# Performance work log

Hardware: AMD Instinct MI355X
Metric: run time of the kernel (lower is better)

## Reference

```python
import jax, jax.numpy as jnp
import numpy as np

N, E = 50000, 800000
IN, H = 128, 128
NTYPE, NSCHOOL, NTIME, NAUTHOR = 20, 30, 15, 200


def setup_inputs() -> dict:
    key = jax.random.key(0)
    ks = jax.random.split(key, 20)

    def lin(k, i, o):  # kaiming-ish init
        return jax.random.normal(k, (i, o), jnp.float32) * (1.0 / np.sqrt(i))

    return {
        "x0": jax.random.normal(ks[0], (N, IN), jnp.float32),
        "edge_index": jax.random.randint(ks[1], (2, E), 0, N, dtype=jnp.int64),
        # GCNConv weights (x @ W + b after aggregation)
        "W1": lin(ks[2], IN, H),   "b1": jnp.zeros((H,), jnp.float32),
        "Wt": lin(ks[3], H, NTYPE),    "bt": jnp.zeros((NTYPE,), jnp.float32),
        "Ws": lin(ks[4], H, NSCHOOL), "bs": jnp.zeros((NSCHOOL,), jnp.float32),
        "Wa": lin(ks[5], H, NAUTHOR), "ba": jnp.zeros((NAUTHOR,), jnp.float32),
        # classification heads (Linear stored as [in, out])
        "Wct": lin(ks[6], NTYPE, NTYPE),       "bct": jnp.zeros((NTYPE,), jnp.float32),
        "Wcs": lin(ks[7], NSCHOOL, NSCHOOL), "bcs": jnp.zeros((NSCHOOL,), jnp.float32),
        "Wtf": lin(ks[8], IN, NTIME),          "btf": jnp.zeros((NTIME,), jnp.float32),
        "Wca": lin(ks[9], NAUTHOR, NAUTHOR), "bca": jnp.zeros((NAUTHOR,), jnp.float32),
    }


def reference(x0, edge_index, W1, b1, Wt, bt, Ws, bs, Wa, ba,
              Wct, bct, Wcs, bcs, Wtf, btf, Wca, bca):
    n = x0.shape[0]
    src, dst = edge_index[0], edge_index[1]
    # GCNConv default: add self-loops, symmetric deg^{-1/2} normalization
    loop = jnp.arange(n, dtype=edge_index.dtype)
    src_f = jnp.concatenate([src, loop])  # [E+N]
    dst_f = jnp.concatenate([dst, loop])
    deg = jax.ops.segment_sum(jnp.ones(src_f.shape[0], jnp.float32), dst_f, num_segments=n)
    dinv = jnp.where(deg > 0, jax.lax.rsqrt(deg), 0.0)
    norm = dinv[src_f] * dinv[dst_f]  # [E+N]

    def conv(x, W, b):
        xt = x @ W                                   # transform first (small out dim)
        msg = xt[src_f] * norm[:, None]              # [E+N, out]
        return jax.ops.segment_sum(msg, dst_f, num_segments=n) + b

    h = jax.nn.relu(conv(x0, W1, b1))  # dropout is identity at inference

    out_type = jax.nn.softmax(conv(h, Wt, bt) @ Wct + bct, axis=-1)
    out_school = jax.nn.softmax(conv(h, Ws, bs) @ Wcs + bcs, axis=-1)
    out_time = jax.nn.softmax(x0 @ Wtf + btf, axis=-1)  # head reads x0 directly
    out_author = jax.nn.softmax(conv(h, Wa, ba) @ Wca + bca, axis=-1)
    return (out_type, out_school, out_time, out_author)
```

## Files before the change

kernel.cpp:

```cpp
#include <hip/hip_runtime.h>
#include <math.h>


typedef short short8 __attribute__((ext_vector_type(8)));
typedef float f32x4 __attribute__((ext_vector_type(4)));

#define FILL_CHUNK 2048

static __device__ __forceinline__ unsigned short f2bf(float x) {
  unsigned u = __float_as_uint(x);
  u += 0x7fff + ((u >> 16) & 1);
  return (unsigned short)(u >> 16);
}
static __device__ __forceinline__ unsigned pack2bf(float lo, float hi) {
  return ((unsigned)f2bf(hi) << 16) | (unsigned)f2bf(lo);
}
static __device__ __forceinline__ float bflo(unsigned u) {
  return __uint_as_float(u << 16);
}
static __device__ __forceinline__ float bfhi(unsigned u) {
  return __uint_as_float(u & 0xffff0000u);
}

__global__ __launch_bounds__(256) void k_deg_x(
    const int* __restrict__ dst, int E, int* __restrict__ deg, int rlen) {
  int rng = blockIdx.x & 7;
  int chunk = blockIdx.x >> 3;
  int lo = rng * rlen, hi = lo + rlen;
  int base = chunk * FILL_CHUNK;
  int end = base + FILL_CHUNK;
  if (end > E) end = E;
  for (int e = base + threadIdx.x; e < end; e += 256) {
    int d = dst[e];
    if (d >= lo && d < hi) atomicAdd(&deg[d], 1);
  }
}

__global__ void k_scan1(const int* __restrict__ deg, int n,
                        int* __restrict__ excl, int* __restrict__ bsum) {
  __shared__ int sm[256];
  int i = blockIdx.x * 256 + threadIdx.x;
  int v = (i < n) ? deg[i] : 0;
  sm[threadIdx.x] = v;
  __syncthreads();
#pragma unroll
  for (int o = 1; o < 256; o <<= 1) {
    int t = (threadIdx.x >= o) ? sm[threadIdx.x - o] : 0;
    __syncthreads();
    sm[threadIdx.x] += t;
    __syncthreads();
  }
  if (i < n) excl[i] = sm[threadIdx.x] - v;
  if (threadIdx.x == 255) bsum[blockIdx.x] = sm[255];
}

__global__ void k_scan2(int* __restrict__ bsum, int nb) {
  __shared__ int sm[256];
  int v = (threadIdx.x < nb) ? bsum[threadIdx.x] : 0;
  sm[threadIdx.x] = v;
  __syncthreads();
#pragma unroll
  for (int o = 1; o < 256; o <<= 1) {
    int t = (threadIdx.x >= o) ? sm[threadIdx.x - o] : 0;
    __syncthreads();
    sm[threadIdx.x] += t;
    __syncthreads();
  }
  if (threadIdx.x < nb) bsum[threadIdx.x] = sm[threadIdx.x] - v;
}

__global__ __launch_bounds__(256) void k_finscale(
    const float* __restrict__ X, const int* __restrict__ deg,
    const int* __restrict__ bsum, int* __restrict__ row_off,
    int* __restrict__ cursor, float* __restrict__ dinv,
    unsigned* __restrict__ Y, int n) {
  int p = blockIdx.x * 256 + threadIdx.x;
  if (p >= n * 64) return;
  int row = p >> 6;
  float d = rsqrtf((float)(deg[row] + 1));
  if ((p & 63) == 0) {
    int ro = row_off[row] + bsum[row >> 8];
    row_off[row] = ro;
    cursor[row] = ro;
    dinv[row] = d;
  }
  float2 v = reinterpret_cast<const float2*>(X)[p];
  Y[p] = pack2bf(v.x * d, v.y * d);
}

__global__ __launch_bounds__(256) void k_fill_x(
    const int* __restrict__ src, const int* __restrict__ dst, int E,
    int* __restrict__ cursor, unsigned short* __restrict__ csr, int rlen) {
  int rng = blockIdx.x & 7;
  int chunk = blockIdx.x >> 3;
  int lo = rng * rlen, hi = lo + rlen;
  int base = chunk * FILL_CHUNK;
  int end = base + FILL_CHUNK;
  if (end > E) end = E;
  for (int e = base + threadIdx.x; e < end; e += 256) {
    int d = dst[e];
    if (d >= lo && d < hi) {
      int p = atomicAdd(&cursor[d], 1);
      csr[p] = (unsigned short)src[e];
    }
  }
}

__global__ __launch_bounds__(256) void k_agg(
    const unsigned* __restrict__ Y, unsigned* __restrict__ out,
    const int* __restrict__ row_off, const int* __restrict__ deg,
    const unsigned short* __restrict__ csr, const float* __restrict__ dinv,
    int n) {
  int wave = threadIdx.x >> 6;
  int lane = threadIdx.x & 63;
  int sub = lane >> 5;
  int sl = lane & 31;
  int i = blockIdx.x * 8 + wave * 2 + sub;
  if (i >= n) return;
  int start = row_off[i];
  int cnt = deg[i];
  const uint2* Yv = reinterpret_cast<const uint2*>(Y);
  float a0 = 0.f, a1 = 0.f, a2 = 0.f, a3 = 0.f;
  int j = 0;
  for (; j + 3 < cnt; j += 4) {
    int s0 = csr[start + j];
    int s1 = csr[start + j + 1];
    int s2 = csr[start + j + 2];
    int s3 = csr[start + j + 3];
    uint2 u0 = Yv[(size_t)s0 * 32 + sl];
    uint2 u1 = Yv[(size_t)s1 * 32 + sl];
    uint2 u2 = Yv[(size_t)s2 * 32 + sl];
    uint2 u3 = Yv[(size_t)s3 * 32 + sl];
    a0 += (bflo(u0.x) + bflo(u1.x)) + (bflo(u2.x) + bflo(u3.x));
    a1 += (bfhi(u0.x) + bfhi(u1.x)) + (bfhi(u2.x) + bfhi(u3.x));
    a2 += (bflo(u0.y) + bflo(u1.y)) + (bflo(u2.y) + bflo(u3.y));
    a3 += (bfhi(u0.y) + bfhi(u1.y)) + (bfhi(u2.y) + bfhi(u3.y));
  }
  for (; j < cnt; ++j) {
    int s0 = csr[start + j];
    uint2 u0 = Yv[(size_t)s0 * 32 + sl];
    a0 += bflo(u0.x);
    a1 += bfhi(u0.x);
    a2 += bflo(u0.y);
    a3 += bfhi(u0.y);
  }
  uint2 us = Yv[(size_t)i * 32 + sl];
  float di = dinv[i];
  uint2 r;
  r.x = pack2bf((a0 + bflo(us.x)) * di, (a1 + bfhi(us.x)) * di);
  r.y = pack2bf((a2 + bflo(us.y)) * di, (a3 + bfhi(us.y)) * di);
  reinterpret_cast<uint2*>(out)[(size_t)i * 32 + sl] = r;
}

__global__ void k_fusepack(
    const float* __restrict__ Wt, const float* __restrict__ bt,
    const float* __restrict__ Wct, const float* __restrict__ bct,
    const float* __restrict__ Ws, const float* __restrict__ bs,
    const float* __restrict__ Wcs, const float* __restrict__ bcs,
    const float* __restrict__ Wa, const float* __restrict__ ba,
    const float* __restrict__ Wca, const float* __restrict__ bca,
    unsigned short* __restrict__ WfPk, float* __restrict__ bf,
    const float* __restrict__ W1, unsigned short* __restrict__ W1Pk) {
  if (blockIdx.x >= 256) {
    int t = (blockIdx.x - 256) * 128 + threadIdx.x;
    int i = t >> 7, c = t & 127;
    W1Pk[((i >> 3) * 128 + c) * 8 + (i & 7)] = f2bf(W1[t]);
    return;
  }
  int c = blockIdx.x;
  int i = threadIdx.x;
  float acc = 0.f, bacc = 0.f;
  if (c < 20) {
    for (int k = 0; k < 20; ++k) {
      float w2 = Wct[k * 20 + c];
      acc += Wt[i * 20 + k] * w2;
      bacc += bt[k] * w2;
    }
    bacc += bct[c];
  } else if (c < 50) {
    int cc = c - 20;
    for (int k = 0; k < 30; ++k) {
      float w2 = Wcs[k * 30 + cc];
      acc += Ws[i * 30 + k] * w2;
      bacc += bs[k] * w2;
    }
    bacc += bcs[cc];
  } else if (c < 250) {
    int cc = c - 50;
    for (int k = 0; k < 200; ++k) {
      float w2 = Wca[k * 200 + cc];
      acc += Wa[i * 200 + k] * w2;
      bacc += ba[k] * w2;
    }
    bacc += bca[cc];
  }
  WfPk[((i >> 3) * 256 + c) * 8 + (i & 7)] = f2bf(acc);
  if (i == 0) bf[c] = bacc;
}

static __device__ __forceinline__ void stage32(
    const short* __restrict__ A, short (*sAb)[136], int rowBase, int n, int tid) {
  for (int t = tid; t < 32 * 16; t += 256) {
    int r = t >> 4, c8 = t & 15;
    int gr = rowBase + r;
    short8 v = (short8){0, 0, 0, 0, 0, 0, 0, 0};
    if (gr < n) v = *reinterpret_cast<const short8*>(A + (size_t)gr * 128 + c8 * 8);
    *reinterpret_cast<short8*>(&sAb[r][c8 * 8]) = v;
  }
}

__global__ __launch_bounds__(256) void k_mfma_gemm128(
    const short* __restrict__ A, const unsigned short* __restrict__ Wpk,
    const float* __restrict__ bias, const float* __restrict__ dinv,
    unsigned short* __restrict__ out, int n) {
  __shared__ short sAb[32][136];
  int rowBase = blockIdx.x * 32;
  stage32(A, sAb, rowBase, n, threadIdx.x);
  __syncthreads();
  int wave = threadIdx.x >> 6, lane = threadIdx.x & 63;
  int rg = wave >> 1, ch = wave & 1;
  int lr = lane & 15, lg = lane >> 4;
  int r0 = rowBase + rg * 16;
  short8 afr[4];
#pragma unroll
  for (int kk = 0; kk < 4; ++kk)
    afr[kk] = *reinterpret_cast<const short8*>(&sAb[rg * 16 + lr][kk * 32 + lg * 8]);
  f32x4 acc[4];
#pragma unroll
  for (int t = 0; t < 4; ++t) acc[t] = (f32x4){0.f, 0.f, 0.f, 0.f};
  const short8* Wp8 = reinterpret_cast<const short8*>(Wpk);
#pragma unroll
  for (int t = 0; t < 4; ++t) {
#pragma unroll
    for (int kk = 0; kk < 4; ++kk) {
      short8 bfr = Wp8[(kk * 4 + lg) * 128 + ch * 64 + t * 16 + lr];
      acc[t] = __builtin_amdgcn_mfma_f32_16x16x32_bf16(afr[kk], bfr, acc[t], 0, 0, 0);
    }
  }
  int rloc = r0 + lg * 4;
#pragma unroll
  for (int t = 0; t < 4; ++t) {
    int col = ch * 64 + t * 16 + lr;
    float b = bias[col];
#pragma unroll
    for (int reg = 0; reg < 4; ++reg) {
      int row = rloc + reg;
      if (row < n) {
        float v = fmaxf(acc[t][reg] + b, 0.f) * dinv[row];
        out[(size_t)row * 128 + col] = f2bf(v);
      }
    }
  }
}

__global__ __launch_bounds__(256) void k_heads_fused(
    const short* __restrict__ A, const unsigned short* __restrict__ Wpk,
    const float* __restrict__ bf, float* __restrict__ outT,
    float* __restrict__ outS, float* __restrict__ outA, int n) {
  __shared__ short sAb[32][136];
  __shared__ float aM[2][2][16];
  __shared__ float aS[2][2][16];
  int rowBase = blockIdx.x * 32;
  stage32(A, sAb, rowBase, n, threadIdx.x);
  __syncthreads();
  int wave = threadIdx.x >> 6, lane = threadIdx.x & 63;
  int rg = wave >> 1, ch = wave & 1;
  int lr = lane & 15, lg = lane >> 4;
  int r0 = rowBase + rg * 16;
  int cb = ch * 128;
  short8 afr[4];
#pragma unroll
  for (int kk = 0; kk < 4; ++kk)
    afr[kk] = *reinterpret_cast<const short8*>(&sAb[rg * 16 + lr][kk * 32 + lg * 8]);
  f32x4 acc[8];
#pragma unroll
  for (int t = 0; t < 8; ++t) acc[t] = (f32x4){0.f, 0.f, 0.f, 0.f};
  const short8* Wp8 = reinterpret_cast<const short8*>(Wpk);
#pragma unroll
  for (int t = 0; t < 8; ++t) {
#pragma unroll
    for (int kk = 0; kk < 4; ++kk) {
      short8 bfr = Wp8[(kk * 4 + lg) * 256 + cb + t * 16 + lr];
      acc[t] = __builtin_amdgcn_mfma_f32_16x16x32_bf16(afr[kk], bfr, acc[t], 0, 0, 0);
    }
  }
  float bias_l[8];
#pragma unroll
  for (int t = 0; t < 8; ++t) bias_l[t] = bf[cb + t * 16 + lr];
  float mTr[4], mSr[4], mAr[4];
#pragma unroll
  for (int reg = 0; reg < 4; ++reg) {
    float mT = -INFINITY, mS = -INFINITY, mA = -INFINITY;
#pragma unroll
    for (int t = 0; t < 8; ++t) {
      int c = cb + t * 16 + lr;
      float val = acc[t][reg] + bias_l[t];
      acc[t][reg] = val;
      if (c < 20) mT = fmaxf(mT, val);
      else if (c < 50) mS = fmaxf(mS, val);
      else if (c < 250) mA = fmaxf(mA, val);
    }
#pragma unroll
    for (int o = 8; o; o >>= 1) {
      mT = fmaxf(mT, __shfl_xor(mT, o, 64));
      mS = fmaxf(mS, __shfl_xor(mS, o, 64));
      mA = fmaxf(mA, __shfl_xor(mA, o, 64));
    }
    mTr[reg] = mT; mSr[reg] = mS; mAr[reg] = mA;
    if (lr == 0) aM[rg][ch][lg * 4 + reg] = mA;
  }
  __syncthreads();
#pragma unroll
  for (int reg = 0; reg < 4; ++reg)
    mAr[reg] = fmaxf(mAr[reg], aM[rg][ch ^ 1][lg * 4 + reg]);
  float sTr[4], sSr[4], sAr[4];
#pragma unroll
  for (int reg = 0; reg < 4; ++reg) {
    float sT = 0.f, sS = 0.f, sA = 0.f;
#pragma unroll
    for (int t = 0; t < 8; ++t) {
      int c = cb + t * 16 + lr;
      float m = (c < 20) ? mTr[reg] : (c < 50) ? mSr[reg] : mAr[reg];
      float e = __expf(acc[t][reg] - m);
      acc[t][reg] = e;
      if (c < 20) sT += e;
      else if (c < 50) sS += e;
      else if (c < 250) sA += e;
    }
#pragma unroll
    for (int o = 8; o; o >>= 1) {
      sT += __shfl_xor(sT, o, 64);
      sS += __shfl_xor(sS, o, 64);
      sA += __shfl_xor(sA, o, 64);
    }
    sTr[reg] = sT; sSr[reg] = sS; sAr[reg] = sA;
    if (lr == 0) aS[rg][ch][lg * 4 + reg] = sA;
  }
  __syncthreads();
#pragma unroll
  for (int reg = 0; reg < 4; ++reg)
    sAr[reg] += aS[rg][ch ^ 1][lg * 4 + reg];
  int rloc = r0 + lg * 4;
#pragma unroll
  for (int reg = 0; reg < 4; ++reg) {
    int row = rloc + reg;
    if (row >= n) continue;
    float iT = 1.f / sTr[reg], iS = 1.f / sSr[reg], iA = 1.f / sAr[reg];
#pragma unroll
    for (int t = 0; t < 8; ++t) {
      int c = cb + t * 16 + lr;
      float e = acc[t][reg];
      if (c < 20) outT[(size_t)row * 20 + c] = e * iT;
      else if (c < 50) outS[(size_t)row * 30 + (c - 20)] = e * iS;
      else if (c < 250) outA[(size_t)row * 200 + (c - 50)] = e * iA;
    }
  }
}

__global__ __launch_bounds__(256) void k_time(
    const float* __restrict__ x0, const float* __restrict__ Wtf,
    const float* __restrict__ btf, float* __restrict__ outT, int n) {
  __shared__ float sW[128][16];
  __shared__ float sb[16];
  for (int t = threadIdx.x; t < 128 * 16; t += 256) {
    int k = t >> 4, j = t & 15;
    sW[k][j] = (j < 15) ? Wtf[k * 15 + j] : 0.f;
  }
  if (threadIdx.x < 16) sb[threadIdx.x] = (threadIdx.x < 15) ? btf[threadIdx.x] : 0.f;
  __syncthreads();
  int j = threadIdx.x & 15;
  int rl = threadIdx.x >> 4;
  int r = blockIdx.x * 16 + rl;
  if (r >= n) return;
  float acc = sb[j];
  const float4* xr = reinterpret_cast<const float4*>(x0 + (size_t)r * 128);
  for (int k4 = 0; k4 < 32; ++k4) {
    float4 xv = xr[k4];
    acc += xv.x * sW[k4 * 4 + 0][j] + xv.y * sW[k4 * 4 + 1][j] +
           xv.z * sW[k4 * 4 + 2][j] + xv.w * sW[k4 * 4 + 3][j];
  }
  float m = (j < 15) ? acc : -INFINITY;
#pragma unroll
  for (int o = 8; o; o >>= 1) m = fmaxf(m, __shfl_xor(m, o, 16));
  float e = (j < 15) ? __expf(acc - m) : 0.f;
  float s = e;
#pragma unroll
  for (int o = 8; o; o >>= 1) s += __shfl_xor(s, o, 16);
  if (j < 15) outT[(size_t)r * 15 + j] = e / s;
}

extern "C" void kernel_launch(void* const* d_in, const int* in_sizes, int n_in,
                              void* d_out, int out_size, void* d_ws, size_t ws_size,
                              hipStream_t stream) {
  const float* x0 = (const float*)d_in[0];
  const int* ei = (const int*)d_in[1];
  const float* W1 = (const float*)d_in[2];
  const float* b1 = (const float*)d_in[3];
  const float* Wt = (const float*)d_in[4];
  const float* bt = (const float*)d_in[5];
  const float* Ws = (const float*)d_in[6];
  const float* bs = (const float*)d_in[7];
  const float* Wa = (const float*)d_in[8];
  const float* ba = (const float*)d_in[9];
  const float* Wct = (const float*)d_in[10];
  const float* bct = (const float*)d_in[11];
  const float* Wcs = (const float*)d_in[12];
  const float* bcs = (const float*)d_in[13];
  const float* Wtf = (const float*)d_in[14];
  const float* btf = (const float*)d_in[15];
  const float* Wca = (const float*)d_in[16];
  const float* bca = (const float*)d_in[17];
  (void)n_in; (void)out_size; (void)ws_size;

  int N = in_sizes[0] / 128;
  int E = in_sizes[1] / 2;
  float* out = (float*)d_out;

  char* ws = (char*)d_ws;
  size_t off = 0;
  auto alloc = [&](size_t bytes) -> void* {
    void* p = ws + off;
    off = (off + bytes + 255) & ~(size_t)255;
    return p;
  };
  int* deg = (int*)alloc((size_t)N * 4);
  int* row_off = (int*)alloc((size_t)N * 4);
  int* bsum = (int*)alloc(256 * 4);
  int* cursor = (int*)alloc((size_t)N * 4);
  float* dinv = (float*)alloc((size_t)N * 4);
  unsigned short* csr = (unsigned short*)alloc((size_t)E * 2);
  unsigned short* WfPk = (unsigned short*)alloc((size_t)128 * 256 * 2);
  unsigned short* W1Pk = (unsigned short*)alloc((size_t)128 * 128 * 2);
  float* bf = (float*)alloc(256 * 4);
  unsigned* Yb = (unsigned*)alloc((size_t)N * 64 * 4);
  unsigned* Ab = (unsigned*)alloc((size_t)N * 64 * 4);
  unsigned* Bb = (unsigned*)alloc((size_t)N * 64 * 4);

  const int* srcp = ei;
  const int* dstp = ei + E;
  int gN = (N + 255) / 256;
  int g32 = (N + 31) / 32;
  int rlen = (N + 7) / 8;
  int gX = 8 * ((E + FILL_CHUNK - 1) / FILL_CHUNK);

  hipMemsetAsync(deg, 0, (size_t)N * 4, stream);
  k_deg_x<<<gX, 256, 0, stream>>>(dstp, E, deg, rlen);
  k_scan1<<<gN, 256, 0, stream>>>(deg, N, row_off, bsum);
  k_scan2<<<1, 256, 0, stream>>>(bsum, gN);
  k_finscale<<<(N * 64 + 255) / 256, 256, 0, stream>>>(
      x0, deg, bsum, row_off, cursor, dinv, Yb, N);
  k_fill_x<<<gX, 256, 0, stream>>>(srcp, dstp, E, cursor, csr, rlen);
  k_fusepack<<<384, 128, 0, stream>>>(Wt, bt, Wct, bct, Ws, bs, Wcs, bcs, Wa, ba,
                                      Wca, bca, WfPk, bf, W1, W1Pk);
  k_agg<<<(N + 7) / 8, 256, 0, stream>>>(Yb, Ab, row_off, deg, csr, dinv, N);
  k_mfma_gemm128<<<g32, 256, 0, stream>>>(
      (const short*)Ab, W1Pk, b1, dinv, (unsigned short*)Bb, N);
  k_agg<<<(N + 7) / 8, 256, 0, stream>>>(Bb, Ab, row_off, deg, csr, dinv, N);
  k_heads_fused<<<g32, 256, 0, stream>>>(
      (const short*)Ab, WfPk, bf, out, out + (size_t)N * 20, out + (size_t)N * 65, N);
  k_time<<<(N + 15) / 16, 256, 0, stream>>>(x0, Wtf, btf, out + (size_t)N * 50, N);
}
```

Before: 336.8 us.

## Fuse neighbor aggregation into GEMM kernels, merge time head, simplify CSR build

The sparse aggregation now writes straight into the shared-memory A tile of the following MFMA GEMM and heads kernels, so the intermediate aggregated feature buffer no longer goes through global memory and two launches are dropped. The time-head softmax runs as extra blocks of the heads kernel and reads Wtf directly instead of staging it in LDS. The range-partitioned degree and fill kernels are replaced by simple one-thread-per-edge atomic kernels. Each GEMM block now does 32 rows of irregular gathers before its MFMA phase, which may lower latency hiding. Unpartitioned atomics may also contend more or lose locality.

```diff
diff --git a/kernel.cpp b/kernel.cpp
--- a/kernel.cpp
+++ b/kernel.cpp
@@ -4,8 +4,6 @@
 
 typedef short short8 __attribute__((ext_vector_type(8)));
 typedef float f32x4 __attribute__((ext_vector_type(4)));
-
-#define FILL_CHUNK 2048
 
 static __device__ __forceinline__ unsigned short f2bf(float x) {
   unsigned u = __float_as_uint(x);
@@ -22,18 +20,9 @@
   return __uint_as_float(u & 0xffff0000u);
 }
 
-__global__ __launch_bounds__(256) void k_deg_x(
-    const int* __restrict__ dst, int E, int* __restrict__ deg, int rlen) {
-  int rng = blockIdx.x & 7;
-  int chunk = blockIdx.x >> 3;
-  int lo = rng * rlen, hi = lo + rlen;
-  int base = chunk * FILL_CHUNK;
-  int end = base + FILL_CHUNK;
-  if (end > E) end = E;
-  for (int e = base + threadIdx.x; e < end; e += 256) {
-    int d = dst[e];
-    if (d >= lo && d < hi) atomicAdd(&deg[d], 1);
-  }
+__global__ void k_deg(const int* __restrict__ dst, int E, int* __restrict__ deg) {
+  int e = blockIdx.x * blockDim.x + threadIdx.x;
+  if (e < E) atomicAdd(&deg[dst[e]], 1);
 }
 
 __global__ void k_scan1(const int* __restrict__ deg, int n,
@@ -88,68 +77,15 @@
   Y[p] = pack2bf(v.x * d, v.y * d);
 }
 
-__global__ __launch_bounds__(256) void k_fill_x(
-    const int* __restrict__ src, const int* __restrict__ dst, int E,
-    int* __restrict__ cursor, unsigned short* __restrict__ csr, int rlen) {
-  int rng = blockIdx.x & 7;
-  int chunk = blockIdx.x >> 3;
-  int lo = rng * rlen, hi = lo + rlen;
-  int base = chunk * FILL_CHUNK;
-  int end = base + FILL_CHUNK;
-  if (end > E) end = E;
-  for (int e = base + threadIdx.x; e < end; e += 256) {
+__global__ void k_fill(const int* __restrict__ src, const int* __restrict__ dst,
+                       int E, int* __restrict__ cursor,
+                       unsigned short* __restrict__ csr) {
+  int e = blockIdx.x * blockDim.x + threadIdx.x;
+  if (e < E) {
     int d = dst[e];
-    if (d >= lo && d < hi) {
-      int p = atomicAdd(&cursor[d], 1);
-      csr[p] = (unsigned short)src[e];
-    }
-  }
-}
-
-__global__ __launch_bounds__(256) void k_agg(
-    const unsigned* __restrict__ Y, unsigned* __restrict__ out,
-    const int* __restrict__ row_off, const int* __restrict__ deg,
-    const unsigned short* __restrict__ csr, const float* __restrict__ dinv,
-    int n) {
-  int wave = threadIdx.x >> 6;
-  int lane = threadIdx.x & 63;
-  int sub = lane >> 5;
-  int sl = lane & 31;
-  int i = blockIdx.x * 8 + wave * 2 + sub;
-  if (i >= n) return;
-  int start = row_off[i];
-  int cnt = deg[i];
-  const uint2* Yv = reinterpret_cast<const uint2*>(Y);
-  float a0 = 0.f, a1 = 0.f, a2 = 0.f, a3 = 0.f;
-  int j = 0;
-  for (; j + 3 < cnt; j += 4) {
-    int s0 = csr[start + j];
-    int s1 = csr[start + j + 1];
-    int s2 = csr[start + j + 2];
-    int s3 = csr[start + j + 3];
-    uint2 u0 = Yv[(size_t)s0 * 32 + sl];
-    uint2 u1 = Yv[(size_t)s1 * 32 + sl];
-    uint2 u2 = Yv[(size_t)s2 * 32 + sl];
-    uint2 u3 = Yv[(size_t)s3 * 32 + sl];
-    a0 += (bflo(u0.x) + bflo(u1.x)) + (bflo(u2.x) + bflo(u3.x));
-    a1 += (bfhi(u0.x) + bfhi(u1.x)) + (bfhi(u2.x) + bfhi(u3.x));
-    a2 += (bflo(u0.y) + bflo(u1.y)) + (bflo(u2.y) + bflo(u3.y));
-    a3 += (bfhi(u0.y) + bfhi(u1.y)) + (bfhi(u2.y) + bfhi(u3.y));
-  }
-  for (; j < cnt; ++j) {
-    int s0 = csr[start + j];
-    uint2 u0 = Yv[(size_t)s0 * 32 + sl];
-    a0 += bflo(u0.x);
-    a1 += bfhi(u0.x);
-    a2 += bflo(u0.y);
-    a3 += bfhi(u0.y);
-  }
-  uint2 us = Yv[(size_t)i * 32 + sl];
-  float di = dinv[i];
-  uint2 r;
-  r.x = pack2bf((a0 + bflo(us.x)) * di, (a1 + bfhi(us.x)) * di);
-  r.y = pack2bf((a2 + bflo(us.y)) * di, (a3 + bfhi(us.y)) * di);
-  reinterpret_cast<uint2*>(out)[(size_t)i * 32 + sl] = r;
+    int p = atomicAdd(&cursor[d], 1);
+    csr[p] = (unsigned short)src[e];
+  }
 }
 
 __global__ void k_fusepack(
@@ -198,24 +134,66 @@
   if (i == 0) bf[c] = bacc;
 }
 
-static __device__ __forceinline__ void stage32(
-    const short* __restrict__ A, short (*sAb)[136], int rowBase, int n, int tid) {
-  for (int t = tid; t < 32 * 16; t += 256) {
-    int r = t >> 4, c8 = t & 15;
-    int gr = rowBase + r;
-    short8 v = (short8){0, 0, 0, 0, 0, 0, 0, 0};
-    if (gr < n) v = *reinterpret_cast<const short8*>(A + (size_t)gr * 128 + c8 * 8);
-    *reinterpret_cast<short8*>(&sAb[r][c8 * 8]) = v;
-  }
-}
-
-__global__ __launch_bounds__(256) void k_mfma_gemm128(
-    const short* __restrict__ A, const unsigned short* __restrict__ Wpk,
-    const float* __restrict__ bias, const float* __restrict__ dinv,
-    unsigned short* __restrict__ out, int n) {
+static __device__ __forceinline__ void agg_to_lds(
+    const unsigned* __restrict__ Y, short (*sAb)[136], int rowBase,
+    const int* __restrict__ row_off, const int* __restrict__ deg,
+    const unsigned short* __restrict__ csr, const float* __restrict__ dinv,
+    int n, int tid) {
+  int wave = tid >> 6, lane = tid & 63;
+  int sub = lane >> 5, sl = lane & 31;
+  const uint2* Yv = reinterpret_cast<const uint2*>(Y);
+#pragma unroll
+  for (int it = 0; it < 4; ++it) {
+    int r = wave * 8 + it * 2 + sub;
+    int i = rowBase + r;
+    uint2 rr;
+    if (i < n) {
+      int start = row_off[i];
+      int cnt = deg[i];
+      float a0 = 0.f, a1 = 0.f, a2 = 0.f, a3 = 0.f;
+      int j = 0;
+      for (; j + 3 < cnt; j += 4) {
+        int s0 = csr[start + j];
+        int s1 = csr[start + j + 1];
+        int s2 = csr[start + j + 2];
+        int s3 = csr[start + j + 3];
+        uint2 u0 = Yv[(size_t)s0 * 32 + sl];
+        uint2 u1 = Yv[(size_t)s1 * 32 + sl];
+        uint2 u2 = Yv[(size_t)s2 * 32 + sl];
+        uint2 u3 = Yv[(size_t)s3 * 32 + sl];
+        a0 += (bflo(u0.x) + bflo(u1.x)) + (bflo(u2.x) + bflo(u3.x));
+        a1 += (bfhi(u0.x) + bfhi(u1.x)) + (bfhi(u2.x) + bfhi(u3.x));
+        a2 += (bflo(u0.y) + bflo(u1.y)) + (bflo(u2.y) + bflo(u3.y));
+        a3 += (bfhi(u0.y) + bfhi(u1.y)) + (bfhi(u2.y) + bfhi(u3.y));
+      }
+      for (; j < cnt; ++j) {
+        int s0 = csr[start + j];
+        uint2 u0 = Yv[(size_t)s0 * 32 + sl];
+        a0 += bflo(u0.x);
+        a1 += bfhi(u0.x);
+        a2 += bflo(u0.y);
+        a3 += bfhi(u0.y);
+      }
+      uint2 us = Yv[(size_t)i * 32 + sl];
+      float di = dinv[i];
+      rr.x = pack2bf((a0 + bflo(us.x)) * di, (a1 + bfhi(us.x)) * di);
+      rr.y = pack2bf((a2 + bflo(us.y)) * di, (a3 + bfhi(us.y)) * di);
+    } else {
+      rr.x = 0u;
+      rr.y = 0u;
+    }
+    *reinterpret_cast<uint2*>(&sAb[r][sl * 4]) = rr;
+  }
+}
+
+__global__ __launch_bounds__(256) void k_agg_gemm128(
+    const unsigned* __restrict__ Y, const int* __restrict__ row_off,
+    const int* __restrict__ deg, const unsigned short* __restrict__ csr,
+    const float* __restrict__ dinv, const unsigned short* __restrict__ Wpk,
+    const float* __restrict__ bias, unsigned short* __restrict__ out, int n) {
   __shared__ short sAb[32][136];
   int rowBase = blockIdx.x * 32;
-  stage32(A, sAb, rowBase, n, threadIdx.x);
+  agg_to_lds(Y, sAb, rowBase, row_off, deg, csr, dinv, n, threadIdx.x);
   __syncthreads();
   int wave = threadIdx.x >> 6, lane = threadIdx.x & 63;
   int rg = wave >> 1, ch = wave & 1;
@@ -253,15 +231,44 @@
   }
 }
 
-__global__ __launch_bounds__(256) void k_heads_fused(
-    const short* __restrict__ A, const unsigned short* __restrict__ Wpk,
-    const float* __restrict__ bf, float* __restrict__ outT,
-    float* __restrict__ outS, float* __restrict__ outA, int n) {
+__global__ __launch_bounds__(256) void k_agg_heads_time(
+    const unsigned* __restrict__ Y, const int* __restrict__ row_off,
+    const int* __restrict__ deg, const unsigned short* __restrict__ csr,
+    const float* __restrict__ dinv, const unsigned short* __restrict__ Wpk,
+    const float* __restrict__ bfb, const float* __restrict__ x0,
+    const float* __restrict__ Wtf, const float* __restrict__ btf,
+    float* __restrict__ outT, float* __restrict__ outS,
+    float* __restrict__ outTime, float* __restrict__ outA, int n) {
+  int g32 = (n + 31) / 32;
+  if ((int)blockIdx.x >= g32) {
+    int tb = blockIdx.x - g32;
+    int j = threadIdx.x & 15;
+    int rl = threadIdx.x >> 4;
+    int r = tb * 16 + rl;
+    if (r >= n) return;
+    int jj = (j < 15) ? j : 14;
+    float acc = btf[jj];
+    const float4* xr = reinterpret_cast<const float4*>(x0 + (size_t)r * 128);
+    for (int k4 = 0; k4 < 32; ++k4) {
+      float4 xv = xr[k4];
+      acc += xv.x * Wtf[(k4 * 4 + 0) * 15 + jj] + xv.y * Wtf[(k4 * 4 + 1) * 15 + jj] +
+             xv.z * Wtf[(k4 * 4 + 2) * 15 + jj] + xv.w * Wtf[(k4 * 4 + 3) * 15 + jj];
+    }
+    float m = (j < 15) ? acc : -INFINITY;
+#pragma unroll
+    for (int o = 8; o; o >>= 1) m = fmaxf(m, __shfl_xor(m, o, 16));
+    float e = (j < 15) ? __expf(acc - m) : 0.f;
+    float s = e;
+#pragma unroll
+    for (int o = 8; o; o >>= 1) s += __shfl_xor(s, o, 16);
+    if (j < 15) outTime[(size_t)r * 15 + j] = e / s;
+    return;
+  }
   __shared__ short sAb[32][136];
   __shared__ float aM[2][2][16];
   __shared__ float aS[2][2][16];
   int rowBase = blockIdx.x * 32;
-  stage32(A, sAb, rowBase, n, threadIdx.x);
+  agg_to_lds(Y, sAb, rowBase, row_off, deg, csr, dinv, n, threadIdx.x);
   __syncthreads();
   int wave = threadIdx.x >> 6, lane = threadIdx.x & 63;
   int rg = wave >> 1, ch = wave & 1;
@@ -286,7 +293,7 @@
   }
   float bias_l[8];
 #pragma unroll
-  for (int t = 0; t < 8; ++t) bias_l[t] = bf[cb + t * 16 + lr];
+  for (int t = 0; t < 8; ++t) bias_l[t] = bfb[cb + t * 16 + lr];
   float mTr[4], mSr[4], mAr[4];
 #pragma unroll
   for (int reg = 0; reg < 4; ++reg) {
@@ -355,38 +362,6 @@
       else if (c < 250) outA[(size_t)row * 200 + (c - 50)] = e * iA;
     }
   }
-}
-
-__global__ __launch_bounds__(256) void k_time(
-    const float* __restrict__ x0, const float* __restrict__ Wtf,
-    const float* __restrict__ btf, float* __restrict__ outT, int n) {
-  __shared__ float sW[128][16];
-  __shared__ float sb[16];
-  for (int t = threadIdx.x; t < 128 * 16; t += 256) {
-    int k = t >> 4, j = t & 15;
-    sW[k][j] = (j < 15) ? Wtf[k * 15 + j] : 0.f;
-  }
-  if (threadIdx.x < 16) sb[threadIdx.x] = (threadIdx.x < 15) ? btf[threadIdx.x] : 0.f;
-  __syncthreads();
-  int j = threadIdx.x & 15;
-  int rl = threadIdx.x >> 4;
-  int r = blockIdx.x * 16 + rl;
-  if (r >= n) return;
-  float acc = sb[j];
-  const float4* xr = reinterpret_cast<const float4*>(x0 + (size_t)r * 128);
-  for (int k4 = 0; k4 < 32; ++k4) {
-    float4 xv = xr[k4];
-    acc += xv.x * sW[k4 * 4 + 0][j] + xv.y * sW[k4 * 4 + 1][j] +
-           xv.z * sW[k4 * 4 + 2][j] + xv.w * sW[k4 * 4 + 3][j];
-  }
-  float m = (j < 15) ? acc : -INFINITY;
-#pragma unroll
-  for (int o = 8; o; o >>= 1) m = fmaxf(m, __shfl_xor(m, o, 16));
-  float e = (j < 15) ? __expf(acc - m) : 0.f;
-  float s = e;
-#pragma unroll
-  for (int o = 8; o; o >>= 1) s += __shfl_xor(s, o, 16);
-  if (j < 15) outT[(size_t)r * 15 + j] = e / s;
 }
 
 extern "C" void kernel_launch(void* const* d_in, const int* in_sizes, int n_in,
@@ -431,32 +406,29 @@
   unsigned short* csr = (unsigned short*)alloc((size_t)E * 2);
   unsigned short* WfPk = (unsigned short*)alloc((size_t)128 * 256 * 2);
   unsigned short* W1Pk = (unsigned short*)alloc((size_t)128 * 128 * 2);
-  float* bf = (float*)alloc(256 * 4);
+  float* bfb = (float*)alloc(256 * 4);
   unsigned* Yb = (unsigned*)alloc((size_t)N * 64 * 4);
-  unsigned* Ab = (unsigned*)alloc((size_t)N * 64 * 4);
   unsigned* Bb = (unsigned*)alloc((size_t)N * 64 * 4);
 
   const int* srcp = ei;
   const int* dstp = ei + E;
+  int gE = (E + 255) / 256;
   int gN = (N + 255) / 256;
   int g32 = (N + 31) / 32;
-  int rlen = (N + 7) / 8;
-  int gX = 8 * ((E + FILL_CHUNK - 1) / FILL_CHUNK);
+  int gT = (N + 15) / 16;
 
   hipMemsetAsync(deg, 0, (size_t)N * 4, stream);
-  k_deg_x<<<gX, 256, 0, stream>>>(dstp, E, deg, rlen);
+  k_deg<<<gE, 256, 0, stream>>>(dstp, E, deg);
   k_scan1<<<gN, 256, 0, stream>>>(deg, N, row_off, bsum);
   k_scan2<<<1, 256, 0, stream>>>(bsum, gN);
   k_finscale<<<(N * 64 + 255) / 256, 256, 0, stream>>>(
       x0, deg, bsum, row_off, cursor, dinv, Yb, N);
-  k_fill_x<<<gX, 256, 0, stream>>>(srcp, dstp, E, cursor, csr, rlen);
+  k_fill<<<gE, 256, 0, stream>>>(srcp, dstp, E, cursor, csr);
   k_fusepack<<<384, 128, 0, stream>>>(Wt, bt, Wct, bct, Ws, bs, Wcs, bcs, Wa, ba,
-                                      Wca, bca, WfPk, bf, W1, W1Pk);
-  k_agg<<<(N + 7) / 8, 256, 0, stream>>>(Yb, Ab, row_off, deg, csr, dinv, N);
-  k_mfma_gemm128<<<g32, 256, 0, stream>>>(
-      (const short*)Ab, W1Pk, b1, dinv, (unsigned short*)Bb, N);
-  k_agg<<<(N + 7) / 8, 256, 0, stream>>>(Bb, Ab, row_off, deg, csr, dinv, N);
-  k_heads_fused<<<g32, 256, 0, stream>>>(
-      (const short*)Ab, WfPk, bf, out, out + (size_t)N * 20, out + (size_t)N * 65, N);
-  k_time<<<(N + 15) / 16, 256, 0, stream>>>(x0, Wtf, btf, out + (size_t)N * 50, N);
-}
+                                      Wca, bca, WfPk, bfb, W1, W1Pk);
+  k_agg_gemm128<<<g32, 256, 0, stream>>>(Yb, row_off, deg, csr, dinv, W1Pk, b1,
+                                         (unsigned short*)Bb, N);
+  k_agg_heads_time<<<g32 + gT, 256, 0, stream>>>(
+      Bb, row_off, deg, csr, dinv, WfPk, bfb, x0, Wtf, btf,
+      out, out + (size_t)N * 20, out + (size_t)N * 50, out + (size_t)N * 65, N);
+}
```

After: 337.1 us. About the same (+0.1%).
